# Performance work log

Hardware: AMD Instinct MI355X
Metric: run time of the kernel (lower is better)

Reference implementation:

```python
import jax, jax.numpy as jnp
import numpy as np

N_NODES = 100000
N_EDGES = 1600000
IN_DIM = 128
HEADS = 4
OUT_DIM = 32
NEG_SLOPE = 0.2  # PyG GATConv default negative_slope


def setup_inputs() -> dict:
    key = jax.random.key(0)
    k_x, k_e, k_w, k_as, k_ad = jax.random.split(key, 5)
    x = jax.random.normal(k_x, (N_NODES, IN_DIM), dtype=jnp.float32)
    edge_index = jax.random.randint(k_e, (2, N_EDGES), 0, N_NODES, dtype=jnp.int64)
    # Glorot-style init for learned parameters (GATConv lin + attention vectors)
    W = jax.random.normal(k_w, (IN_DIM, HEADS * OUT_DIM), dtype=jnp.float32) / np.sqrt(IN_DIM)
    att_src = jax.random.normal(k_as, (HEADS, OUT_DIM), dtype=jnp.float32) / np.sqrt(OUT_DIM)
    att_dst = jax.random.normal(k_ad, (HEADS, OUT_DIM), dtype=jnp.float32) / np.sqrt(OUT_DIM)
    bias = jnp.zeros((HEADS * OUT_DIM,), dtype=jnp.float32)
    return {"x": x, "edge_index": edge_index, "W": W, "att_src": att_src,
            "att_dst": att_dst, "bias": bias}


def reference(x, edge_index, W, att_src, att_dst, bias):
    N = x.shape[0]
    H, D = att_src.shape
    # PyG GATConv default: add self loops
    loop = jnp.arange(N, dtype=edge_index.dtype)
    src = jnp.concatenate([edge_index[0], loop])  # message sources  [E+N]
    dst = jnp.concatenate([edge_index[1], loop])  # message targets  [E+N]

    h = (x @ W).reshape(N, H, D)                          # [N, H, D]
    a_src = jnp.einsum('nhd,hd->nh', h, att_src)          # [N, H]
    a_dst = jnp.einsum('nhd,hd->nh', h, att_dst)          # [N, H]

    # per-edge attention logits, LeakyReLU(neg_slope=0.2)
    e = jax.nn.leaky_relu(a_src[src] + a_dst[dst], NEG_SLOPE)  # [E+N, H]

    # segment softmax over edges grouped by target node (numerically stable)
    e_max = jax.ops.segment_max(e, dst, num_segments=N)        # [N, H]
    e_max = jnp.where(jnp.isfinite(e_max), e_max, jnp.float32(0))
    ex = jnp.exp(e - e_max[dst])                               # [E+N, H]
    denom = jax.ops.segment_sum(ex, dst, num_segments=N)       # [N, H]
    alpha = ex / (denom[dst] + jnp.float32(1e-16))             # [E+N, H]

    # weighted scatter-aggregate of source features
    msg = h[src] * alpha[:, :, None]                           # [E+N, H, D]
    out = jax.ops.segment_sum(msg, dst, num_segments=N)        # [N, H, D]
    out = out.reshape(N, H * D) + bias                         # concat heads + bias
    return jax.nn.elu(out)                                     # wrapper ELU
```

## Files before the change

kernel.cpp:

```cpp
#include <hip/hip_runtime.h>
#include <hip/hip_fp16.h>
#include <math.h>

#define N_NODES 100000
#define N_EDGES 1600000
#define IN_DIM 128
#define F_DIM 128
#define NEG_SLOPE 0.2f

#define BUCKW_LOG 7
#define NBUCK 784
#define NBLK 800
#define EPB 2000
#define G_TOT (NBUCK * NBLK)
#define SC_CHUNK 4096
#define SC_NB ((G_TOT + SC_CHUNK - 1) / SC_CHUNK)
#define CSR_CAP (N_EDGES + NBUCK * 384)

typedef short v8s __attribute__((ext_vector_type(8)));
typedef float v4f __attribute__((ext_vector_type(4)));

static __device__ __forceinline__ unsigned short f2bf(float f) {
    unsigned u = __float_as_uint(f);
    u += 0x7fffu + ((u >> 16) & 1u);
    return (unsigned short)(u >> 16);
}
static __device__ __forceinline__ float bf2f(unsigned s) { return __uint_as_float(s << 16); }

__global__ __launch_bounds__(256) void k_wprep(const float* __restrict__ W,
                                               unsigned short* __restrict__ Wt) {
    int i = blockIdx.x * 256 + threadIdx.x;
    int n = i >> 7, k = i & 127;
    Wt[n * 128 + k] = f2bf(W[k * 128 + n]);
}

__global__ __launch_bounds__(256) void k_gemm(const float* __restrict__ x,
                                              const unsigned short* __restrict__ Wt,
                                              unsigned short* __restrict__ h16,
                                              const float* __restrict__ att_src,
                                              const float* __restrict__ att_dst,
                                              float* __restrict__ a_src,
                                              float* __restrict__ a_dst) {
    __shared__ unsigned short As[64][136];
    __shared__ unsigned short Bs[128][136];
    __shared__ float attl[256];
    const int t  = threadIdx.x;
    const int n0 = blockIdx.x * 64;

    attl[t] = (t < 128) ? att_src[t] : att_dst[t - 128];

    {
        int row = t >> 2, k0 = (t & 3) * 32;
        int n = n0 + row;
        #pragma unroll
        for (int i = 0; i < 4; i++) {
            float4 va = make_float4(0.f,0.f,0.f,0.f), vb = va;
            if (n < N_NODES) {
                const float* p = x + (size_t)n * IN_DIM + k0 + i * 8;
                va = *(const float4*)p;
                vb = *(const float4*)(p + 4);
            }
            uint4 u;
            u.x = f2bf(va.x) | ((unsigned)f2bf(va.y) << 16);
            u.y = f2bf(va.z) | ((unsigned)f2bf(va.w) << 16);
            u.z = f2bf(vb.x) | ((unsigned)f2bf(vb.y) << 16);
            u.w = f2bf(vb.z) | ((unsigned)f2bf(vb.w) << 16);
            *(uint4*)&As[row][k0 + i * 8] = u;
        }
    }
    {
        int nr = t >> 1, s0 = (t & 1) * 64;
        const uint4* src = (const uint4*)(Wt + nr * 128 + s0);
        #pragma unroll
        for (int i = 0; i < 8; i++)
            *(uint4*)&Bs[nr][s0 + i * 8] = src[i];
    }
    __syncthreads();

    const int w = t >> 6, lane = t & 63;
    const int mr = lane & 15, quad = lane >> 4;
    const int m0 = w * 16;

    v4f acc[8];
    #pragma unroll
    for (int nt = 0; nt < 8; nt++) acc[nt] = (v4f){0.f, 0.f, 0.f, 0.f};

    #pragma unroll
    for (int kk = 0; kk < 4; kk++) {
        int kof = kk * 32 + quad * 8;
        v8s a = *(const v8s*)&As[m0 + mr][kof];
        #pragma unroll
        for (int nt = 0; nt < 8; nt++) {
            v8s b = *(const v8s*)&Bs[nt * 16 + mr][kof];
            acc[nt] = __builtin_amdgcn_mfma_f32_16x16x32_bf16(a, b, acc[nt], 0, 0, 0);
        }
    }

    #pragma unroll
    for (int nt = 0; nt < 8; nt++)
        #pragma unroll
        for (int r = 0; r < 4; r++)
            As[m0 + quad * 4 + r][nt * 16 + mr] = f2bf(acc[nt][r]);
    __syncthreads();
    {
        int row = m0 + (lane >> 2);
        int c0  = (lane & 3) * 32;
        int n = n0 + row;
        if (n < N_NODES) {
            float ds = 0.f, dd = 0.f;
            #pragma unroll
            for (int i = 0; i < 4; i++) {
                uint4 v = *(const uint4*)&As[row][c0 + i * 8];
                *(uint4*)&h16[(size_t)n * F_DIM + c0 + i * 8] = v;
                float f0 = bf2f(v.x & 0xffffu), f1 = bf2f(v.x >> 16);
                float f2 = bf2f(v.y & 0xffffu), f3 = bf2f(v.y >> 16);
                float f4 = bf2f(v.z & 0xffffu), f5 = bf2f(v.z >> 16);
                float f6 = bf2f(v.w & 0xffffu), f7 = bf2f(v.w >> 16);
                const float* ps = &attl[c0 + i * 8];
                const float* pd = &attl[128 + c0 + i * 8];
                ds += f0*ps[0] + f1*ps[1] + f2*ps[2] + f3*ps[3]
                    + f4*ps[4] + f5*ps[5] + f6*ps[6] + f7*ps[7];
                dd += f0*pd[0] + f1*pd[1] + f2*pd[2] + f3*pd[3]
                    + f4*pd[4] + f5*pd[5] + f6*pd[6] + f7*pd[7];
            }
            int hd = lane & 3;
            a_src[n * 4 + hd] = ds;
            a_dst[n * 4 + hd] = dd;
        }
    }
}

__global__ __launch_bounds__(256) void k_bhist(const int* __restrict__ ei_dst,
                                               int* __restrict__ G) {
    __shared__ int hist[NBUCK];
    for (int i = threadIdx.x; i < NBUCK; i += 256) hist[i] = 0;
    __syncthreads();
    int e0 = blockIdx.x * EPB;
    for (int i = threadIdx.x; i < EPB; i += 256) {
        int d = ei_dst[e0 + i];
        atomicAdd(&hist[d >> BUCKW_LOG], 1);
    }
    __syncthreads();
    for (int b = threadIdx.x; b < NBUCK; b += 256)
        G[b * NBLK + blockIdx.x] = hist[b];
}

__global__ __launch_bounds__(256) void k_scanp(const int* __restrict__ a,
                                               int* __restrict__ part) {
    int base = blockIdx.x * SC_CHUNK + threadIdx.x * 16;
    int s = 0;
    #pragma unroll
    for (int i = 0; i < 16; i++) {
        int idx = base + i;
        if (idx < G_TOT) s += a[idx];
    }
    __shared__ int wsum[4];
    for (int off = 32; off >= 1; off >>= 1) s += __shfl_down(s, off, 64);
    if ((threadIdx.x & 63) == 0) wsum[threadIdx.x >> 6] = s;
    __syncthreads();
    if (threadIdx.x == 0) part[blockIdx.x] = wsum[0] + wsum[1] + wsum[2] + wsum[3];
}

__global__ void k_scant(int* part, int* boff) {
    if (blockIdx.x == 0 && threadIdx.x == 0) {
        int run = 0;
        for (int b = 0; b < SC_NB; b++) { int v = part[b]; part[b] = run; run += v; }
        boff[NBUCK] = N_EDGES;
    }
}

__global__ __launch_bounds__(256) void k_scand(int* __restrict__ a,
                                               const int* __restrict__ part,
                                               int* __restrict__ boff) {
    __shared__ int tsum[256];
    int tid  = threadIdx.x;
    int base = blockIdx.x * SC_CHUNK + tid * 16;
    int v[16]; int s = 0;
    #pragma unroll
    for (int i = 0; i < 16; i++) {
        int idx = base + i;
        v[i] = (idx < G_TOT) ? a[idx] : 0;
        s += v[i];
    }
    tsum[tid] = s;
    __syncthreads();
    for (int off = 1; off < 256; off <<= 1) {
        int y = (tid >= off) ? tsum[tid - off] : 0;
        __syncthreads();
        tsum[tid] += y;
        __syncthreads();
    }
    int run = part[blockIdx.x] + tsum[tid] - s;
    #pragma unroll
    for (int i = 0; i < 16; i++) {
        int idx = base + i;
        if (idx < G_TOT) {
            a[idx] = run;
            if (idx % NBLK == 0) boff[idx / NBLK] = run;
        }
        run += v[i];
    }
}

__global__ __launch_bounds__(256) void k_bscat(const int* __restrict__ ei,
                                               const int* __restrict__ G,
                                               int* __restrict__ ebuf) {
    __shared__ int base[NBUCK];
    for (int b = threadIdx.x; b < NBUCK; b += 256)
        base[b] = G[b * NBLK + blockIdx.x];
    __syncthreads();
    int e0 = blockIdx.x * EPB;
    for (int i = threadIdx.x; i < EPB; i += 256) {
        int s = ei[e0 + i];
        int d = ei[N_EDGES + e0 + i];
        int b = d >> BUCKW_LOG;
        int pos = atomicAdd(&base[b], 1);
        ebuf[pos] = s | ((d & 127) << 17);
    }
}

__global__ __launch_bounds__(256) void k_csrfin(const int* __restrict__ ebuf,
                                                const int* __restrict__ boff,
                                                const float* __restrict__ a_src,
                                                const float* __restrict__ a_dst,
                                                int* __restrict__ ebeg,
                                                int* __restrict__ eend,
                                                int* __restrict__ csr2,
                                                __half* __restrict__ pbuf) {
    __shared__ int cnt[128];
    __shared__ int off[128];
    int b = blockIdx.x;
    int beg = boff[b], end = boff[b + 1];
    int padded_base = beg + b * 384;
    if (threadIdx.x < 128) cnt[threadIdx.x] = 0;
    __syncthreads();
    for (int j = beg + threadIdx.x; j < end; j += 256)
        atomicAdd(&cnt[(ebuf[j] >> 17) & 127], 1);
    __syncthreads();
    if (threadIdx.x == 0) {
        int run = padded_base;
        for (int i = 0; i < 128; i++) { off[i] = run; run += (cnt[i] + 3) & ~3; }
    }
    __syncthreads();
    if (threadIdx.x < 128) {
        int node = (b << BUCKW_LOG) + threadIdx.x;
        int c = cnt[threadIdx.x];
        if (node < N_NODES) {
            ebeg[node] = off[threadIdx.x];
            eend[node] = off[threadIdx.x] + c;
            int cpad = (c + 3) & ~3;
            for (int k = c; k < cpad; k++) {
                int pos = off[threadIdx.x] + k;
                csr2[pos] = node;
                *(uint2*)&pbuf[(size_t)pos * 4] = make_uint2(0u, 0u);
            }
        }
        cnt[threadIdx.x] = 0;
    }
    __syncthreads();
    for (int j = beg + threadIdx.x; j < end; j += 256) {
        int p = ebuf[j];
        int dl = (p >> 17) & 127;
        int s = p & 0x1ffff;
        int r = atomicAdd(&cnt[dl], 1);
        int pos = off[dl] + r;
        csr2[pos] = s;
        int d = (b << BUCKW_LOG) + dl;
        float4 as = *(const float4*)&a_src[s * 4];
        float4 ad = *(const float4*)&a_dst[d * 4];
        float e0 = as.x + ad.x; e0 = e0 > 0.f ? e0 : NEG_SLOPE * e0;
        float e1 = as.y + ad.y; e1 = e1 > 0.f ? e1 : NEG_SLOPE * e1;
        float e2 = as.z + ad.z; e2 = e2 > 0.f ? e2 : NEG_SLOPE * e2;
        float e3 = as.w + ad.w; e3 = e3 > 0.f ? e3 : NEG_SLOPE * e3;
        __half2 lo = __floats2half2_rn(__expf(e0), __expf(e1));
        __half2 hi = __floats2half2_rn(__expf(e2), __expf(e3));
        *(uint2*)&pbuf[(size_t)pos * 4] =
            make_uint2(*(unsigned*)&lo, *(unsigned*)&hi);
    }
}

__global__ __launch_bounds__(256) void k_agg(const uint4* __restrict__ h16x4,
                                             const float* __restrict__ a_src,
                                             const float* __restrict__ a_dst,
                                             const int* __restrict__ ebeg,
                                             const int* __restrict__ eend,
                                             const int* __restrict__ csr2,
                                             const __half* __restrict__ pbuf,
                                             const float* __restrict__ bias,
                                             float* __restrict__ out) {
    int n = (blockIdx.x * 256 + threadIdx.x) >> 6;
    if (n >= N_NODES) return;
    int lane = threadIdx.x & 63;
    int grp = lane >> 4, g = lane & 15, hd = g >> 2;

    float p0 = 0.f;
    if (grp == 0) {
        float e0 = a_src[n * 4 + hd] + a_dst[n * 4 + hd];
        e0 = e0 > 0.f ? e0 : NEG_SLOPE * e0;
        p0 = __expf(e0);
    }
    uint4 hs = h16x4[(size_t)n * 16 + g];
    float l  = p0;
    float a0 = p0 * bf2f(hs.x & 0xffffu), a1 = p0 * bf2f(hs.x >> 16);
    float a2 = p0 * bf2f(hs.y & 0xffffu), a3 = p0 * bf2f(hs.y >> 16);
    float a4 = p0 * bf2f(hs.z & 0xffffu), a5 = p0 * bf2f(hs.z >> 16);
    float a6 = p0 * bf2f(hs.w & 0xffffu), a7 = p0 * bf2f(hs.w >> 16);

    int beg = ebeg[n], cnt = eend[n] - beg;
    const int* sp = csr2 + beg + grp;
    const __half* pp = pbuf + (size_t)(beg + grp) * 4 + hd;
    int steps = (cnt + 3) >> 2;
    int t = 0;
    for (; t + 2 <= steps; t += 2) {
        int s0 = sp[4 * t];
        int s1 = sp[4 * t + 4];
        float q0 = __half2float(pp[16 * t]);
        float q1 = __half2float(pp[16 * t + 16]);
        uint4 h0 = h16x4[(size_t)s0 * 16 + g];
        uint4 h1 = h16x4[(size_t)s1 * 16 + g];
        l  += q0 + q1;
        a0 += q0 * bf2f(h0.x & 0xffffu) + q1 * bf2f(h1.x & 0xffffu);
        a1 += q0 * bf2f(h0.x >> 16)     + q1 * bf2f(h1.x >> 16);
        a2 += q0 * bf2f(h0.y & 0xffffu) + q1 * bf2f(h1.y & 0xffffu);
        a3 += q0 * bf2f(h0.y >> 16)     + q1 * bf2f(h1.y >> 16);
        a4 += q0 * bf2f(h0.z & 0xffffu) + q1 * bf2f(h1.z & 0xffffu);
        a5 += q0 * bf2f(h0.z >> 16)     + q1 * bf2f(h1.z >> 16);
        a6 += q0 * bf2f(h0.w & 0xffffu) + q1 * bf2f(h1.w & 0xffffu);
        a7 += q0 * bf2f(h0.w >> 16)     + q1 * bf2f(h1.w >> 16);
    }
    if (t < steps) {
        int s0 = sp[4 * t];
        float q0 = __half2float(pp[16 * t]);
        uint4 h0 = h16x4[(size_t)s0 * 16 + g];
        l  += q0;
        a0 += q0 * bf2f(h0.x & 0xffffu);
        a1 += q0 * bf2f(h0.x >> 16);
        a2 += q0 * bf2f(h0.y & 0xffffu);
        a3 += q0 * bf2f(h0.y >> 16);
        a4 += q0 * bf2f(h0.z & 0xffffu);
        a5 += q0 * bf2f(h0.z >> 16);
        a6 += q0 * bf2f(h0.w & 0xffffu);
        a7 += q0 * bf2f(h0.w >> 16);
    }
    #define RED2(v) v += __shfl_xor(v, 16, 64); v += __shfl_xor(v, 32, 64);
    RED2(l); RED2(a0); RED2(a1); RED2(a2); RED2(a3);
    RED2(a4); RED2(a5); RED2(a6); RED2(a7);
    #undef RED2

    if (grp == 0) {
        float inv = 1.f / (l + 1e-16f);
        float4 b0 = *(const float4*)&bias[g * 8];
        float4 b1 = *(const float4*)&bias[g * 8 + 4];
        float o0 = a0 * inv + b0.x, o1 = a1 * inv + b0.y;
        float o2 = a2 * inv + b0.z, o3 = a3 * inv + b0.w;
        float o4 = a4 * inv + b1.x, o5 = a5 * inv + b1.y;
        float o6 = a6 * inv + b1.z, o7 = a7 * inv + b1.w;
        o0 = o0 > 0.f ? o0 : expm1f(o0);
        o1 = o1 > 0.f ? o1 : expm1f(o1);
        o2 = o2 > 0.f ? o2 : expm1f(o2);
        o3 = o3 > 0.f ? o3 : expm1f(o3);
        o4 = o4 > 0.f ? o4 : expm1f(o4);
        o5 = o5 > 0.f ? o5 : expm1f(o5);
        o6 = o6 > 0.f ? o6 : expm1f(o6);
        o7 = o7 > 0.f ? o7 : expm1f(o7);
        *(float4*)&out[(size_t)n * F_DIM + g * 8]     = make_float4(o0, o1, o2, o3);
        *(float4*)&out[(size_t)n * F_DIM + g * 8 + 4] = make_float4(o4, o5, o6, o7);
    }
}

extern "C" void kernel_launch(void* const* d_in, const int* in_sizes, int n_in,
                              void* d_out, int out_size, void* d_ws, size_t ws_size,
                              hipStream_t stream) {
    const float* x       = (const float*)d_in[0];
    const int*   ei      = (const int*)d_in[1];
    const float* W       = (const float*)d_in[2];
    const float* att_src = (const float*)d_in[3];
    const float* att_dst = (const float*)d_in[4];
    const float* bias    = (const float*)d_in[5];
    float*       out     = (float*)d_out;

    char* ws = (char*)d_ws;
    unsigned short* h16 = (unsigned short*)ws; ws += (size_t)N_NODES * F_DIM * 2;
    unsigned short* Wt  = (unsigned short*)ws; ws += (size_t)IN_DIM * F_DIM * 2;
    float* a_src  = (float*)ws; ws += (size_t)N_NODES * 4 * 4;
    float* a_dst  = (float*)ws; ws += (size_t)N_NODES * 4 * 4;
    int*   G      = (int*)ws;   ws += (size_t)G_TOT * 4;
    int*   part   = (int*)ws;   ws += 1024;
    int*   boff   = (int*)ws;   ws += 4096;
    int*   ebeg   = (int*)ws;   ws += (size_t)N_NODES * 4 + 512;
    int*   eend   = (int*)ws;   ws += (size_t)N_NODES * 4 + 512;
    int*   ebuf   = (int*)ws;   ws += (size_t)N_EDGES * 4;
    int*   csr2   = (int*)ws;   ws += (size_t)CSR_CAP * 4;
    __half* pbuf  = (__half*)ws; ws += (size_t)CSR_CAP * 4 * 2;

    k_wprep<<<64, 256, 0, stream>>>(W, Wt);
    k_gemm<<<(N_NODES + 63) / 64, 256, 0, stream>>>(x, Wt, h16, att_src, att_dst, a_src, a_dst);

    k_bhist<<<NBLK, 256, 0, stream>>>(ei + N_EDGES, G);
    k_scanp<<<SC_NB, 256, 0, stream>>>(G, part);
    k_scant<<<1, 64, 0, stream>>>(part, boff);
    k_scand<<<SC_NB, 256, 0, stream>>>(G, part, boff);
    k_bscat<<<NBLK, 256, 0, stream>>>(ei, G, ebuf);
    k_csrfin<<<NBUCK, 256, 0, stream>>>(ebuf, boff, a_src, a_dst, ebeg, eend, csr2, pbuf);

    k_agg<<<(N_NODES * 64 + 255) / 256, 256, 0, stream>>>((const uint4*)h16, a_src, a_dst, ebeg, eend, csr2, pbuf, bias, out);
}
```

Measured before the change: 302.0 us.

## Shrink bucket-sort grid, warp-parallel scan, cheaper bf16 unpack, packed edge bounds

Cuts the bucket histogram/scatter grid from 800 to 128 blocks with larger per-block edge chunks. This shrinks the global histogram array and the prefix-scan work. The single-thread serial partial-sum scan becomes a 64-lane shuffle scan, which only works because the partial count now fits in one wavefront. Also unpacks bf16 high halves with a mask instead of a shift, merges begin/end edge offsets into one int2 load, and computes ELU with a fast exp minus one. Risks are fewer blocks leaving CUs idle in the scatter phases, and slightly less accurate ELU for small negatives.

Result: no change. 301.1 us (-0.3%).

```diff
diff --git a/kernel.cpp b/kernel.cpp
--- a/kernel.cpp
+++ b/kernel.cpp
@@ -10,8 +10,8 @@
 
 #define BUCKW_LOG 7
 #define NBUCK 784
-#define NBLK 800
-#define EPB 2000
+#define NBLK 128
+#define EPB 12500
 #define G_TOT (NBUCK * NBLK)
 #define SC_CHUNK 4096
 #define SC_NB ((G_TOT + SC_CHUNK - 1) / SC_CHUNK)
@@ -26,6 +26,8 @@
     return (unsigned short)(u >> 16);
 }
 static __device__ __forceinline__ float bf2f(unsigned s) { return __uint_as_float(s << 16); }
+static __device__ __forceinline__ float lo2f(unsigned u) { return __uint_as_float(u << 16); }
+static __device__ __forceinline__ float hi2f(unsigned u) { return __uint_as_float(u & 0xffff0000u); }
 
 __global__ __launch_bounds__(256) void k_wprep(const float* __restrict__ W,
                                                unsigned short* __restrict__ Wt) {
@@ -112,10 +114,10 @@
             for (int i = 0; i < 4; i++) {
                 uint4 v = *(const uint4*)&As[row][c0 + i * 8];
                 *(uint4*)&h16[(size_t)n * F_DIM + c0 + i * 8] = v;
-                float f0 = bf2f(v.x & 0xffffu), f1 = bf2f(v.x >> 16);
-                float f2 = bf2f(v.y & 0xffffu), f3 = bf2f(v.y >> 16);
-                float f4 = bf2f(v.z & 0xffffu), f5 = bf2f(v.z >> 16);
-                float f6 = bf2f(v.w & 0xffffu), f7 = bf2f(v.w >> 16);
+                float f0 = lo2f(v.x), f1 = hi2f(v.x);
+                float f2 = lo2f(v.y), f3 = hi2f(v.y);
+                float f4 = lo2f(v.z), f5 = hi2f(v.z);
+                float f6 = lo2f(v.w), f7 = hi2f(v.w);
                 const float* ps = &attl[c0 + i * 8];
                 const float* pd = &attl[128 + c0 + i * 8];
                 ds += f0*ps[0] + f1*ps[1] + f2*ps[2] + f3*ps[3]
@@ -162,11 +164,16 @@
 }
 
 __global__ void k_scant(int* part, int* boff) {
-    if (blockIdx.x == 0 && threadIdx.x == 0) {
-        int run = 0;
-        for (int b = 0; b < SC_NB; b++) { int v = part[b]; part[b] = run; run += v; }
-        boff[NBUCK] = N_EDGES;
-    }
+    int lane = threadIdx.x & 63;
+    int v = (lane < SC_NB) ? part[lane] : 0;
+    int x = v;
+    #pragma unroll
+    for (int off = 1; off < 64; off <<= 1) {
+        int y = __shfl_up(x, off, 64);
+        if (lane >= off) x += y;
+    }
+    if (lane < SC_NB) part[lane] = x - v;
+    if (lane == 0) boff[NBUCK] = N_EDGES;
 }
 
 __global__ __launch_bounds__(256) void k_scand(int* __restrict__ a,
@@ -223,8 +230,7 @@
                                                 const int* __restrict__ boff,
                                                 const float* __restrict__ a_src,
                                                 const float* __restrict__ a_dst,
-                                                int* __restrict__ ebeg,
-                                                int* __restrict__ eend,
+                                                int2* __restrict__ ebounds,
                                                 int* __restrict__ csr2,
                                                 __half* __restrict__ pbuf) {
     __shared__ int cnt[128];
@@ -246,8 +252,7 @@
         int node = (b << BUCKW_LOG) + threadIdx.x;
         int c = cnt[threadIdx.x];
         if (node < N_NODES) {
-            ebeg[node] = off[threadIdx.x];
-            eend[node] = off[threadIdx.x] + c;
+            ebounds[node] = make_int2(off[threadIdx.x], off[threadIdx.x] + c);
             int cpad = (c + 3) & ~3;
             for (int k = c; k < cpad; k++) {
                 int pos = off[threadIdx.x] + k;
@@ -282,8 +287,7 @@
 __global__ __launch_bounds__(256) void k_agg(const uint4* __restrict__ h16x4,
                                              const float* __restrict__ a_src,
                                              const float* __restrict__ a_dst,
-                                             const int* __restrict__ ebeg,
-                                             const int* __restrict__ eend,
+                                             const int2* __restrict__ ebounds,
                                              const int* __restrict__ csr2,
                                              const __half* __restrict__ pbuf,
                                              const float* __restrict__ bias,
@@ -301,12 +305,13 @@
     }
     uint4 hs = h16x4[(size_t)n * 16 + g];
     float l  = p0;
-    float a0 = p0 * bf2f(hs.x & 0xffffu), a1 = p0 * bf2f(hs.x >> 16);
-    float a2 = p0 * bf2f(hs.y & 0xffffu), a3 = p0 * bf2f(hs.y >> 16);
-    float a4 = p0 * bf2f(hs.z & 0xffffu), a5 = p0 * bf2f(hs.z >> 16);
-    float a6 = p0 * bf2f(hs.w & 0xffffu), a7 = p0 * bf2f(hs.w >> 16);
-
-    int beg = ebeg[n], cnt = eend[n] - beg;
+    float a0 = p0 * lo2f(hs.x), a1 = p0 * hi2f(hs.x);
+    float a2 = p0 * lo2f(hs.y), a3 = p0 * hi2f(hs.y);
+    float a4 = p0 * lo2f(hs.z), a5 = p0 * hi2f(hs.z);
+    float a6 = p0 * lo2f(hs.w), a7 = p0 * hi2f(hs.w);
+
+    int2 eb = ebounds[n];
+    int beg = eb.x, cnt = eb.y - eb.x;
     const int* sp = csr2 + beg + grp;
     const __half* pp = pbuf + (size_t)(beg + grp) * 4 + hd;
     int steps = (cnt + 3) >> 2;
@@ -319,28 +324,28 @@
         uint4 h0 = h16x4[(size_t)s0 * 16 + g];
         uint4 h1 = h16x4[(size_t)s1 * 16 + g];
         l  += q0 + q1;
-        a0 += q0 * bf2f(h0.x & 0xffffu) + q1 * bf2f(h1.x & 0xffffu);
-        a1 += q0 * bf2f(h0.x >> 16)     + q1 * bf2f(h1.x >> 16);
-        a2 += q0 * bf2f(h0.y & 0xffffu) + q1 * bf2f(h1.y & 0xffffu);
-        a3 += q0 * bf2f(h0.y >> 16)     + q1 * bf2f(h1.y >> 16);
-        a4 += q0 * bf2f(h0.z & 0xffffu) + q1 * bf2f(h1.z & 0xffffu);
-        a5 += q0 * bf2f(h0.z >> 16)     + q1 * bf2f(h1.z >> 16);
-        a6 += q0 * bf2f(h0.w & 0xffffu) + q1 * bf2f(h1.w & 0xffffu);
-        a7 += q0 * bf2f(h0.w >> 16)     + q1 * bf2f(h1.w >> 16);
+        a0 += q0 * lo2f(h0.x) + q1 * lo2f(h1.x);
+        a1 += q0 * hi2f(h0.x) + q1 * hi2f(h1.x);
+        a2 += q0 * lo2f(h0.y) + q1 * lo2f(h1.y);
+        a3 += q0 * hi2f(h0.y) + q1 * hi2f(h1.y);
+        a4 += q0 * lo2f(h0.z) + q1 * lo2f(h1.z);
+        a5 += q0 * hi2f(h0.z) + q1 * hi2f(h1.z);
+        a6 += q0 * lo2f(h0.w) + q1 * lo2f(h1.w);
+        a7 += q0 * hi2f(h0.w) + q1 * hi2f(h1.w);
     }
     if (t < steps) {
         int s0 = sp[4 * t];
         float q0 = __half2float(pp[16 * t]);
         uint4 h0 = h16x4[(size_t)s0 * 16 + g];
         l  += q0;
-        a0 += q0 * bf2f(h0.x & 0xffffu);
-        a1 += q0 * bf2f(h0.x >> 16);
-        a2 += q0 * bf2f(h0.y & 0xffffu);
-        a3 += q0 * bf2f(h0.y >> 16);
-        a4 += q0 * bf2f(h0.z & 0xffffu);
-        a5 += q0 * bf2f(h0.z >> 16);
-        a6 += q0 * bf2f(h0.w & 0xffffu);
-        a7 += q0 * bf2f(h0.w >> 16);
+        a0 += q0 * lo2f(h0.x);
+        a1 += q0 * hi2f(h0.x);
+        a2 += q0 * lo2f(h0.y);
+        a3 += q0 * hi2f(h0.y);
+        a4 += q0 * lo2f(h0.z);
+        a5 += q0 * hi2f(h0.z);
+        a6 += q0 * lo2f(h0.w);
+        a7 += q0 * hi2f(h0.w);
     }
     #define RED2(v) v += __shfl_xor(v, 16, 64); v += __shfl_xor(v, 32, 64);
     RED2(l); RED2(a0); RED2(a1); RED2(a2); RED2(a3);
@@ -355,14 +360,14 @@
         float o2 = a2 * inv + b0.z, o3 = a3 * inv + b0.w;
         float o4 = a4 * inv + b1.x, o5 = a5 * inv + b1.y;
         float o6 = a6 * inv + b1.z, o7 = a7 * inv + b1.w;
-        o0 = o0 > 0.f ? o0 : expm1f(o0);
-        o1 = o1 > 0.f ? o1 : expm1f(o1);
-        o2 = o2 > 0.f ? o2 : expm1f(o2);
-        o3 = o3 > 0.f ? o3 : expm1f(o3);
-        o4 = o4 > 0.f ? o4 : expm1f(o4);
-        o5 = o5 > 0.f ? o5 : expm1f(o5);
-        o6 = o6 > 0.f ? o6 : expm1f(o6);
-        o7 = o7 > 0.f ? o7 : expm1f(o7);
+        o0 = o0 > 0.f ? o0 : __expf(o0) - 1.f;
+        o1 = o1 > 0.f ? o1 : __expf(o1) - 1.f;
+        o2 = o2 > 0.f ? o2 : __expf(o2) - 1.f;
+        o3 = o3 > 0.f ? o3 : __expf(o3) - 1.f;
+        o4 = o4 > 0.f ? o4 : __expf(o4) - 1.f;
+        o5 = o5 > 0.f ? o5 : __expf(o5) - 1.f;
+        o6 = o6 > 0.f ? o6 : __expf(o6) - 1.f;
+        o7 = o7 > 0.f ? o7 : __expf(o7) - 1.f;
         *(float4*)&out[(size_t)n * F_DIM + g * 8]     = make_float4(o0, o1, o2, o3);
         *(float4*)&out[(size_t)n * F_DIM + g * 8 + 4] = make_float4(o4, o5, o6, o7);
     }
@@ -387,8 +392,7 @@
     int*   G      = (int*)ws;   ws += (size_t)G_TOT * 4;
     int*   part   = (int*)ws;   ws += 1024;
     int*   boff   = (int*)ws;   ws += 4096;
-    int*   ebeg   = (int*)ws;   ws += (size_t)N_NODES * 4 + 512;
-    int*   eend   = (int*)ws;   ws += (size_t)N_NODES * 4 + 512;
+    int2*  ebounds= (int2*)ws;  ws += (size_t)N_NODES * 8 + 512;
     int*   ebuf   = (int*)ws;   ws += (size_t)N_EDGES * 4;
     int*   csr2   = (int*)ws;   ws += (size_t)CSR_CAP * 4;
     __half* pbuf  = (__half*)ws; ws += (size_t)CSR_CAP * 4 * 2;
@@ -401,7 +405,7 @@
     k_scant<<<1, 64, 0, stream>>>(part, boff);
     k_scand<<<SC_NB, 256, 0, stream>>>(G, part, boff);
     k_bscat<<<NBLK, 256, 0, stream>>>(ei, G, ebuf);
-    k_csrfin<<<NBUCK, 256, 0, stream>>>(ebuf, boff, a_src, a_dst, ebeg, eend, csr2, pbuf);
-
-    k_agg<<<(N_NODES * 64 + 255) / 256, 256, 0, stream>>>((const uint4*)h16, a_src, a_dst, ebeg, eend, csr2, pbuf, bias, out);
-}
+    k_csrfin<<<NBUCK, 256, 0, stream>>>(ebuf, boff, a_src, a_dst, ebounds, csr2, pbuf);
+
+    k_agg<<<(N_NODES * 64 + 255) / 256, 256, 0, stream>>>((const uint4*)h16, a_src, a_dst, ebounds, csr2, pbuf, bias, out);
+}
```
